# Kernel tuning notes

Hardware: AMD Instinct MI355X
Metric: run time of the kernel (lower is better)

The kernel has to match this reference:

```python
import jax, jax.numpy as jnp
import numpy as np

WS = 7          # window size
NH = 8          # num heads
EPS = 1e-5


def _rel_pos_index(ws):
    # timm WindowAttention relative_position_index, shape (ws*ws, ws*ws), values in [0, (2ws-1)^2)
    coords = np.stack(np.meshgrid(np.arange(ws), np.arange(ws), indexing='ij'))  # 2,ws,ws
    coords = coords.reshape(2, -1)
    rel = coords[:, :, None] - coords[:, None, :]          # 2,N,N
    rel = rel.transpose(1, 2, 0)                           # N,N,2
    rel[:, :, 0] += ws - 1
    rel[:, :, 1] += ws - 1
    rel[:, :, 0] *= 2 * ws - 1
    return rel.sum(-1)                                     # N,N

RPI = jnp.asarray(_rel_pos_index(WS), dtype=jnp.int32)


def _ln(x, g, b):
    mu = jnp.mean(x, axis=-1, keepdims=True)
    var = jnp.mean(jnp.square(x - mu), axis=-1, keepdims=True)
    return (x - mu) * jax.lax.rsqrt(var + EPS) * g + b


def setup_inputs() -> dict:
    key = jax.random.key(0)
    ks = jax.random.split(key, 16)
    C, Hd, V = 256, 1024, 7
    s = lambda k, shp, fan: jax.random.normal(k, shp, jnp.float32) * (fan ** -0.5)
    return {
        'x': jax.random.normal(ks[0], (256, 256, 14, 14), jnp.float32),
        'conv_w': s(ks[1], (C, C), C), 'conv_b': jnp.zeros((C,), jnp.float32),
        'ln1_g': jnp.ones((C,), jnp.float32), 'ln1_b': jnp.zeros((C,), jnp.float32),
        'qkv_w': s(ks[2], (C, 3 * C), C), 'qkv_b': jnp.zeros((3 * C,), jnp.float32),
        'rpb': 0.02 * jax.random.normal(ks[3], ((2 * WS - 1) ** 2, NH), jnp.float32),
        'proj_w': s(ks[4], (C, C), C), 'proj_b': jnp.zeros((C,), jnp.float32),
        'ln2_g': jnp.ones((C,), jnp.float32), 'ln2_b': jnp.zeros((C,), jnp.float32),
        'fc1_w': s(ks[5], (C, Hd), C), 'fc1_b': jnp.zeros((Hd,), jnp.float32),
        'fc2_w': s(ks[6], (Hd, C), Hd), 'fc2_b': jnp.zeros((C,), jnp.float32),
        'fc_out_w': s(ks[7], (C, V), C), 'fc_out_b': jnp.zeros((V,), jnp.float32),
    }


def reference(x, conv_w, conv_b, ln1_g, ln1_b, qkv_w, qkv_b, rpb, proj_w, proj_b,
              ln2_g, ln2_b, fc1_w, fc1_b, fc2_w, fc2_b, fc_out_w, fc_out_b):
    B, Cin, H, W = x.shape
    C = conv_w.shape[0]
    hd = C // NH
    # 1x1 conv projection -> tokens (B, H*W, C)
    t = jnp.einsum('oc,bchw->bhwo', conv_w, x) + conv_b            # B,H,W,C
    tok = t.reshape(B, H * W, C)
    # --- Swin block, shift_size=0 ---
    shortcut = tok
    y = _ln(tok, ln1_g, ln1_b).reshape(B, H, W, C)
    # window partition -> (B*nW, ws*ws, C)
    nHw, nWw = H // WS, W // WS
    yw = y.reshape(B, nHw, WS, nWw, WS, C).transpose(0, 1, 3, 2, 4, 5)
    yw = yw.reshape(B * nHw * nWw, WS * WS, C)
    N = WS * WS
    qkv = (yw @ qkv_w + qkv_b).reshape(-1, N, 3, NH, hd).transpose(2, 0, 3, 1, 4)
    q, k, v = qkv[0], qkv[1], qkv[2]                               # (Bn, NH, N, hd)
    attn = jnp.einsum('bhqd,bhkd->bhqk', q * (hd ** -0.5), k)
    attn = attn + rpb[RPI].transpose(2, 0, 1)[None]                # + (NH,N,N) bias
    attn = jax.nn.softmax(attn, axis=-1)
    o = jnp.einsum('bhqk,bhkd->bqhd', attn, v).reshape(-1, N, C)
    o = o @ proj_w + proj_b
    # window reverse
    o = o.reshape(B, nHw, nWw, WS, WS, C).transpose(0, 1, 3, 2, 4, 5).reshape(B, H * W, C)
    tok = shortcut + o                                             # drop_path = identity (eval)
    h = _ln(tok, ln2_g, ln2_b)
    h = jax.nn.gelu(h @ fc1_w + fc1_b, approximate=False) @ fc2_w + fc2_b
    tok = tok + h
    # global average pool over spatial tokens, then classifier
    pooled = jnp.mean(tok, axis=1)                                 # B,C
    return pooled @ fc_out_w + fc_out_b
```

## Files before the change

kernel.cpp:

```cpp
#include <hip/hip_runtime.h>
#include <math.h>

#define NHEADS 8
#define BATCH  256
#define HWTOK  196
#define MTOT   50176

#define BM 128
#define BN 128
#define BK 64

typedef short bfrag8 __attribute__((ext_vector_type(8)));
typedef float ffrag4 __attribute__((ext_vector_type(4)));

__device__ __forceinline__ unsigned short f2bf(float f) {
  union { float f; unsigned u; } v; v.f = f;
  unsigned r = v.u + 0x7fffu + ((v.u >> 16) & 1u);
  return (unsigned short)(r >> 16);
}
__device__ __forceinline__ float bf2f(unsigned short b) {
  union { unsigned u; float f; } v; v.u = ((unsigned)b) << 16;
  return v.f;
}
__device__ __forceinline__ float bflo(unsigned u) {
  union { unsigned x; float f; } v; v.x = u << 16; return v.f;
}
__device__ __forceinline__ float bfhi(unsigned u) {
  union { unsigned x; float f; } v; v.x = u & 0xffff0000u; return v.f;
}
__device__ __forceinline__ unsigned cvtpk(float a, float b) {
  unsigned r;
  asm("v_cvt_pk_bf16_f32 %0, %1, %2" : "=v"(r) : "v"(a), "v"(b));
  return r;
}
__device__ __forceinline__ float gelu_fast(float x) {
  float ax = fabsf(x);
  float z = ax * 0.70710678118654752f;
  float t = __builtin_amdgcn_rcpf(fmaf(z, 0.3275911f, 1.0f));
  float y = t * (0.254829592f +
            t * (-0.284496736f +
            t * (1.421413741f +
            t * (-1.453152027f +
            t * 1.061405429f))));
  float e2 = __expf(-z * z);
  float erfv = fmaf(-y, e2, 1.0f);
  return 0.5f * fmaf(ax, erfv, x);
}
__device__ __forceinline__ int window_reverse_row(int m) {
  int widx = m / 49, pos = m % 49;
  int b = widx >> 2, wh = (widx >> 1) & 1, ww = widx & 1;
  int i = pos / 7, j = pos % 7;
  return b * 196 + (wh * 7 + i) * 14 + (ww * 7 + j);
}

__device__ __forceinline__ void gload16(const void* g, void* l) {
  __builtin_amdgcn_global_load_lds(
      (const __attribute__((address_space(1))) void*)g,
      (__attribute__((address_space(3))) void*)l, 16, 0, 0);
}

template <int EPI>
__global__ __launch_bounds__(256) void k_gemm_mfma(const unsigned short* __restrict__ A,
                                                   const unsigned short* __restrict__ BT,
                                                   const float* __restrict__ bias,
                                                   void* __restrict__ Cout,
                                                   int rowbase, int N, int K, int nNt) {
  __shared__ __align__(128) unsigned short S[16384];
  const int t = threadIdx.x;
  const int lane = t & 63, w = t >> 6;
  const int wr = w >> 1, wc = w & 1;
  const int cpx = gridDim.x >> 3;
  const int lb = (blockIdx.x & 7) * cpx + (blockIdx.x >> 3);
  const int n_t = lb % nNt, m_t = lb / nNt;
  const int m0 = m_t * BM, n0 = n_t * BN;
  const int l15 = lane & 15;
  const int sw = (lane & 7) << 3;
  const int rA = lane >> 3;
  const int kin = (((lane & 7) ^ rA) << 3);
  ffrag4 acc[4][4] = {};

  for (int k0 = 0; k0 < K; k0 += BK) {
#pragma unroll
    for (int i = 0; i < 4; ++i) {
      const int seg = i * 4 + w;
      const int row = seg * 8 + rA;
      gload16(A + (size_t)(m0 + row) * K + k0 + kin, (char*)S + seg * 1024);
      gload16(BT + (size_t)(n0 + row) * K + k0 + kin, (char*)S + 16384 + seg * 1024);
    }
    __syncthreads();
#pragma unroll
    for (int kk = 0; kk < BK; kk += 32) {
      bfrag8 af[4], bfr[4];
      const int colA = (kk + (lane >> 4) * 8) ^ sw;
#pragma unroll
      for (int mi = 0; mi < 4; ++mi) {
        int row = wr * 64 + mi * 16 + l15;
        af[mi] = *(const bfrag8*)&S[row * BK + colA];
      }
#pragma unroll
      for (int ni = 0; ni < 4; ++ni) {
        int col = wc * 64 + ni * 16 + l15;
        bfr[ni] = *(const bfrag8*)&S[8192 + col * BK + colA];
      }
#pragma unroll
      for (int mi = 0; mi < 4; ++mi)
#pragma unroll
        for (int ni = 0; ni < 4; ++ni)
          acc[mi][ni] = __builtin_amdgcn_mfma_f32_16x16x32_bf16(af[mi], bfr[ni], acc[mi][ni], 0, 0, 0);
    }
    __syncthreads();
  }

  const int cr = (lane >> 4) * 4;
  const int cc = l15;
  float bv[4];
#pragma unroll
  for (int ni = 0; ni < 4; ++ni) bv[ni] = bias[n0 + wc * 64 + ni * 16 + cc];

  float* Sf = (float*)S;
#pragma unroll
  for (int pass = 0; pass < 2; ++pass) {
    if (wr == pass) {
#pragma unroll
      for (int mi = 0; mi < 4; ++mi) {
#pragma unroll
        for (int j = 0; j < 4; ++j) {
          const int mloc = mi * 16 + cr + j;
#pragma unroll
          for (int ni = 0; ni < 4; ++ni) {
            const int nl = wc * 64 + ni * 16 + cc;
            float v = acc[mi][ni][j] + bv[ni];
            if (EPI == 1) v = gelu_fast(v);
            Sf[mloc * 128 + nl] = v;
          }
        }
      }
    }
    __syncthreads();
#pragma unroll
    for (int r = 0; r < 4; ++r) {
      const int flat = (r * 256 + t) * 8;
      const int ml = flat >> 7, nl = flat & 127;
      float4 a = *(const float4*)&Sf[flat];
      float4 b2 = *(const float4*)&Sf[flat + 4];
      uint4 o;
      if (EPI == 2 || EPI == 3) {
        const int gm = rowbase + m0 + pass * 64 + ml;
        const int row = (EPI == 2) ? window_reverse_row(gm) : gm;
        unsigned short* dst = (unsigned short*)Cout + (size_t)row * N + n0 + nl;
        uint4 old = *(const uint4*)dst;
        o.x = cvtpk(bflo(old.x) + a.x, bfhi(old.x) + a.y);
        o.y = cvtpk(bflo(old.y) + a.z, bfhi(old.y) + a.w);
        o.z = cvtpk(bflo(old.z) + b2.x, bfhi(old.z) + b2.y);
        o.w = cvtpk(bflo(old.w) + b2.z, bfhi(old.w) + b2.w);
        *(uint4*)dst = o;
      } else {
        o.x = cvtpk(a.x, a.y);  o.y = cvtpk(a.z, a.w);
        o.z = cvtpk(b2.x, b2.y); o.w = cvtpk(b2.z, b2.w);
        *(uint4*)((unsigned short*)Cout + (size_t)(m0 + pass * 64 + ml) * N + n0 + nl) = o;
      }
    }
    if (pass == 0) __syncthreads();
  }
}

__global__ __launch_bounds__(256) void k_wtrans(const float* __restrict__ w,
                                                unsigned short* __restrict__ wt,
                                                int K, int N) {
  __shared__ float tile[32][33];
  int k0 = blockIdx.x * 32, n0 = blockIdx.y * 32;
  int tx = threadIdx.x & 31, ty = threadIdx.x >> 5;
#pragma unroll
  for (int r = 0; r < 4; ++r)
    tile[ty + r * 8][tx] = w[(size_t)(k0 + ty + r * 8) * N + n0 + tx];
  __syncthreads();
#pragma unroll
  for (int r = 0; r < 4; ++r)
    wt[(size_t)(n0 + ty + r * 8) * K + k0 + tx] = f2bf(tile[tx][ty + r * 8]);
}

__global__ __launch_bounds__(256) void k_cast(const float* __restrict__ w,
                                              unsigned short* __restrict__ wb, int n) {
  int i = blockIdx.x * 256 + threadIdx.x;
  if (i < n) wb[i] = f2bf(w[i]);
}

__global__ __launch_bounds__(256) void k_transpose_x(const float* __restrict__ x,
                                                     unsigned short* __restrict__ xt) {
  __shared__ float tile[32][33];
  int b = blockIdx.x;
  int hw0 = blockIdx.y * 32;
  int c0 = blockIdx.z * 32;
  int tx = threadIdx.x & 31, ty = threadIdx.x >> 5;
#pragma unroll
  for (int r = 0; r < 4; ++r) {
    int c = c0 + ty + r * 8, hw = hw0 + tx;
    if (hw < HWTOK) tile[ty + r * 8][tx] = x[((size_t)b * 256 + c) * HWTOK + hw];
  }
  __syncthreads();
#pragma unroll
  for (int r = 0; r < 4; ++r) {
    int hw = hw0 + ty + r * 8, c = c0 + tx;
    if (hw < HWTOK) xt[((size_t)b * HWTOK + hw) * 256 + c] = f2bf(tile[tx][ty + r * 8]);
  }
}

template <bool WINDOW>
__global__ __launch_bounds__(256) void k_layernorm(const unsigned short* __restrict__ in,
                                                   const float* __restrict__ g,
                                                   const float* __restrict__ bta,
                                                   unsigned short* __restrict__ out,
                                                   int rowbase) {
  int wid = threadIdx.x >> 6, lane = threadIdx.x & 63;
  int li = blockIdx.x * 4 + wid;
  int token = rowbase + li;
  const uint2 xr = *(const uint2*)(in + (size_t)token * 256 + lane * 4);
  float x0 = bflo(xr.x), x1 = bfhi(xr.x), x2 = bflo(xr.y), x3 = bfhi(xr.y);
  float s = x0 + x1 + x2 + x3;
  float sq = x0 * x0 + x1 * x1 + x2 * x2 + x3 * x3;
#pragma unroll
  for (int off = 32; off >= 1; off >>= 1) {
    s += __shfl_xor(s, off);
    sq += __shfl_xor(sq, off);
  }
  float mean = s * (1.f / 256.f);
  float var = sq * (1.f / 256.f) - mean * mean;
  float rstd = rsqrtf(var + 1e-5f);
  float4 gv = *(const float4*)(g + lane * 4);
  float4 bv = *(const float4*)(bta + lane * 4);
  uint2 ov;
  ov.x = cvtpk((x0 - mean) * rstd * gv.x + bv.x,
               (x1 - mean) * rstd * gv.y + bv.y);
  ov.y = cvtpk((x2 - mean) * rstd * gv.z + bv.z,
               (x3 - mean) * rstd * gv.w + bv.w);
  int orow;
  if (WINDOW) {
    int b = token / 196, hw = token % 196;
    int h14 = hw / 14, w14 = hw % 14;
    int wh = h14 / 7, i = h14 % 7, ww = w14 / 7, j = w14 % 7;
    int widx = (b * 2 + wh) * 2 + ww;
    orow = widx * 49 + i * 7 + j - rowbase;
  } else {
    orow = li;
  }
  *(uint2*)(out + (size_t)orow * 256 + lane * 4) = ov;
}

__global__ __launch_bounds__(256) void k_attention(const unsigned short* __restrict__ qkv,
                                                   const float* __restrict__ rpb,
                                                   unsigned short* __restrict__ o) {
  __shared__ unsigned short Kl[4][64 * 40];
  __shared__ unsigned short VTl[4][32 * 72];
  __shared__ unsigned short Pl[4][64 * 72];
  __shared__ float rpbl[4][176];

  const int t = threadIdx.x;
  const int w4 = t >> 6, lane = t & 63;
  const int l15 = lane & 15, g = lane >> 4;
  const int gw = blockIdx.x * 4 + w4;
  const int lw = gw >> 3, head = gw & 7;

  unsigned short* K_ = Kl[w4];
  unsigned short* VT_ = VTl[w4];
  unsigned short* P_ = Pl[w4];
  float* rpb_ = rpbl[w4];

  const size_t baseq = (size_t)lw * 49 * 768 + head * 32;

  for (int e = lane; e < 169; e += 64) rpb_[e] = rpb[e * 8 + head];

  for (int e = lane; e < 512; e += 64) {
    int d = e >> 4, tk = 48 + (e & 15);
    if ((e & 15) != 0) VT_[d * 72 + tk] = 0;
  }

  for (int e = lane; e < 784; e += 64) {
    int tok = e >> 4, dp = e & 15;
    unsigned kv = *(const unsigned*)(qkv + baseq + 256 + (size_t)tok * 768 + dp * 2);
    *(unsigned*)&K_[tok * 40 + dp * 2] = kv;
    unsigned vv = *(const unsigned*)(qkv + baseq + 512 + (size_t)tok * 768 + dp * 2);
    VT_[(dp * 2 + 0) * 72 + tok] = (unsigned short)(vv & 0xffffu);
    VT_[(dp * 2 + 1) * 72 + tok] = (unsigned short)(vv >> 16);
  }

  ffrag4 acc[4][4] = {};
  {
    bfrag8 af[4], bfr[4];
#pragma unroll
    for (int qi = 0; qi < 4; ++qi)
      af[qi] = *(const bfrag8*)(qkv + baseq + (size_t)(16 * qi + l15) * 768 + g * 8);
#pragma unroll
    for (int kj = 0; kj < 4; ++kj)
      bfr[kj] = *(const bfrag8*)&K_[(16 * kj + l15) * 40 + g * 8];
#pragma unroll
    for (int qi = 0; qi < 4; ++qi)
#pragma unroll
      for (int kj = 0; kj < 4; ++kj)
        acc[qi][kj] = __builtin_amdgcn_mfma_f32_16x16x32_bf16(af[qi], bfr[kj], acc[qi][kj], 0, 0, 0);
  }

  const float scale = 0.17677669529663687f;
  int kc[4];
  bool kvalid[4];
#pragma unroll
  for (int kj = 0; kj < 4; ++kj) {
    int c = 16 * kj + l15;
    kc[kj] = 13 * (c / 7) + (c % 7);
    kvalid[kj] = (c < 49);
  }
#pragma unroll
  for (int qi = 0; qi < 4; ++qi) {
#pragma unroll
    for (int j = 0; j < 4; ++j) {
      int q = 16 * qi + 4 * g + j;
      int qc = 13 * (q / 7) + (q % 7);
      float tv[4];
#pragma unroll
      for (int kj = 0; kj < 4; ++kj)
        tv[kj] = kvalid[kj] ? (acc[qi][kj][j] * scale + rpb_[qc - kc[kj] + 84]) : -INFINITY;
      float mx = fmaxf(fmaxf(tv[0], tv[1]), fmaxf(tv[2], tv[3]));
#pragma unroll
      for (int off = 8; off >= 1; off >>= 1) mx = fmaxf(mx, __shfl_xor(mx, off));
      float p[4], sum = 0.f;
#pragma unroll
      for (int kj = 0; kj < 4; ++kj) {
        p[kj] = kvalid[kj] ? __expf(tv[kj] - mx) : 0.f;
        sum += p[kj];
      }
#pragma unroll
      for (int off = 8; off >= 1; off >>= 1) sum += __shfl_xor(sum, off);
      float inv = __builtin_amdgcn_rcpf(sum);
      if (q < 49) {
#pragma unroll
        for (int kj = 0; kj < 4; ++kj)
          P_[q * 72 + 16 * kj + l15] = f2bf(p[kj] * inv);
      }
    }
  }

  ffrag4 accO[2][4] = {};
#pragma unroll
  for (int kk = 0; kk < 64; kk += 32) {
    bfrag8 af2[2], bf2[4];
#pragma unroll
    for (int ti = 0; ti < 2; ++ti)
      af2[ti] = *(const bfrag8*)&VT_[(16 * ti + l15) * 72 + kk + g * 8];
#pragma unroll
    for (int qj = 0; qj < 4; ++qj)
      bf2[qj] = *(const bfrag8*)&P_[(16 * qj + l15) * 72 + kk + g * 8];
#pragma unroll
    for (int ti = 0; ti < 2; ++ti)
#pragma unroll
      for (int qj = 0; qj < 4; ++qj)
        accO[ti][qj] = __builtin_amdgcn_mfma_f32_16x16x32_bf16(af2[ti], bf2[qj], accO[ti][qj], 0, 0, 0);
  }

#pragma unroll
  for (int qj = 0; qj < 4; ++qj) {
    int q = 16 * qj + l15;
    if (q < 49) {
#pragma unroll
      for (int ti = 0; ti < 2; ++ti) {
        uint2 ov;
        ov.x = cvtpk(accO[ti][qj][0], accO[ti][qj][1]);
        ov.y = cvtpk(accO[ti][qj][2], accO[ti][qj][3]);
        *(uint2*)(o + ((size_t)lw * 49 + q) * 256 + head * 32 + 16 * ti + 4 * g) = ov;
      }
    }
  }
}

__global__ __launch_bounds__(256) void k_pool(const unsigned short* __restrict__ tok,
                                              float* __restrict__ pooled) {
  int b = blockIdx.x, c = threadIdx.x;
  float s = 0.f;
  for (int hw = 0; hw < 196; ++hw) s += bf2f(tok[((size_t)b * 196 + hw) * 256 + c]);
  pooled[b * 256 + c] = s * (1.f / 196.f);
}

__global__ __launch_bounds__(64) void k_head(const float* __restrict__ pooled,
                                             const float* __restrict__ w,
                                             const float* __restrict__ bias,
                                             float* __restrict__ out) {
  int b = blockIdx.x, t = threadIdx.x;
  if (t < 7) {
    float s = bias[t];
    for (int c = 0; c < 256; ++c) s = fmaf(pooled[b * 256 + c], w[c * 7 + t], s);
    out[b * 7 + t] = s;
  }
}

extern "C" void kernel_launch(void* const* d_in, const int* in_sizes, int n_in,
                              void* d_out, int out_size, void* d_ws, size_t ws_size,
                              hipStream_t stream) {
  const float* x      = (const float*)d_in[0];
  const float* conv_w = (const float*)d_in[1];
  const float* conv_b = (const float*)d_in[2];
  const float* ln1_g  = (const float*)d_in[3];
  const float* ln1_b  = (const float*)d_in[4];
  const float* qkv_w  = (const float*)d_in[5];
  const float* qkv_b  = (const float*)d_in[6];
  const float* rpb    = (const float*)d_in[7];
  const float* proj_w = (const float*)d_in[8];
  const float* proj_b = (const float*)d_in[9];
  const float* ln2_g  = (const float*)d_in[10];
  const float* ln2_b  = (const float*)d_in[11];
  const float* fc1_w  = (const float*)d_in[12];
  const float* fc1_b  = (const float*)d_in[13];
  const float* fc2_w  = (const float*)d_in[14];
  const float* fc2_b  = (const float*)d_in[15];
  const float* fco_w  = (const float*)d_in[16];
  const float* fco_b  = (const float*)d_in[17];
  float* out = (float*)d_out;
  char* p = (char*)d_ws;

  const size_t FULL_NEED = 182000000ull;
  const int nch = (ws_size >= FULL_NEED) ? 1 : 4;
  const int chw = 1024 / nch;
  const size_t chrows = (size_t)chw * 49;
  const int nMt = (int)(chrows / BM);

  unsigned short* tok = (unsigned short*)p;   p += (size_t)MTOT * 256 * 2;
  unsigned short* Bbuf = (unsigned short*)p;  p += chrows * 1024 * 2;
  unsigned short* Abuf = (unsigned short*)p;  p += chrows * 256 * 2;
  unsigned short* Cbuf = (unsigned short*)p;  p += chrows * 256 * 2;
  unsigned short* cwB  = (unsigned short*)p;  p += 65536 * 2;
  unsigned short* qkvT = (unsigned short*)p;  p += 196608 * 2;
  unsigned short* projT= (unsigned short*)p;  p += 65536 * 2;
  unsigned short* fc1T = (unsigned short*)p;  p += 262144 * 2;
  unsigned short* fc2T = (unsigned short*)p;  p += 262144 * 2;
  float* pool = (float*)p;                    p += 65536 * 4;
  unsigned short* xt = Bbuf;

  k_cast<<<256, 256, 0, stream>>>(conv_w, cwB, 65536);
  k_wtrans<<<dim3(8, 24), 256, 0, stream>>>(qkv_w, qkvT, 256, 768);
  k_wtrans<<<dim3(8, 8), 256, 0, stream>>>(proj_w, projT, 256, 256);
  k_wtrans<<<dim3(8, 32), 256, 0, stream>>>(fc1_w, fc1T, 256, 1024);
  k_wtrans<<<dim3(32, 8), 256, 0, stream>>>(fc2_w, fc2T, 1024, 256);

  k_transpose_x<<<dim3(BATCH, 7, 8), 256, 0, stream>>>(x, xt);
  k_gemm_mfma<0><<<(MTOT / BM) * 2, 256, 0, stream>>>(xt, cwB, conv_b, tok, 0, 256, 256, 2);

  for (int c = 0; c < nch; ++c) {
    const int rowbase = c * (int)chrows;
    k_layernorm<true><<<chrows / 4, 256, 0, stream>>>(tok, ln1_g, ln1_b, Abuf, rowbase);
    k_gemm_mfma<0><<<nMt * 6, 256, 0, stream>>>(Abuf, qkvT, qkv_b, Bbuf, 0, 768, 256, 6);
    k_attention<<<chw * 2, 256, 0, stream>>>(Bbuf, rpb, Cbuf);
    k_gemm_mfma<2><<<nMt * 2, 256, 0, stream>>>(Cbuf, projT, proj_b, tok, rowbase, 256, 256, 2);
    k_layernorm<false><<<chrows / 4, 256, 0, stream>>>(tok, ln2_g, ln2_b, Abuf, rowbase);
    k_gemm_mfma<1><<<nMt * 8, 256, 0, stream>>>(Abuf, fc1T, fc1_b, Bbuf, 0, 1024, 256, 8);
    k_gemm_mfma<3><<<nMt * 2, 256, 0, stream>>>(Bbuf, fc2T, fc2_b, tok, rowbase, 256, 1024, 2);
  }

  k_pool<<<BATCH, 256, 0, stream>>>(tok, pool);
  k_head<<<BATCH, 64, 0, stream>>>(pool, fco_w, fco_b, out);
}
```

Before: 307.4 us.

## Double-buffer GEMM LDS tiles with BK=32 to overlap loads and MFMA

Replaces the single-buffered BK=64 K-loop with two BK=32 LDS buffers, prefetching the next slice while MFMAs run on the current one. The LDS swizzle and load mapping change to fit the 32-wide rows. This is meant to hide global-to-LDS latency behind compute and drop one barrier per tile. The cost is a barrier every 32 K instead of every 64, and less work per iteration to cover latency.

```diff
diff --git a/kernel.cpp b/kernel.cpp
--- a/kernel.cpp
+++ b/kernel.cpp
@@ -8,7 +8,6 @@
 
 #define BM 128
 #define BN 128
-#define BK 64
 
 typedef short bfrag8 __attribute__((ext_vector_type(8)));
 typedef float ffrag4 __attribute__((ext_vector_type(4)));
@@ -74,42 +73,52 @@
   const int n_t = lb % nNt, m_t = lb / nNt;
   const int m0 = m_t * BM, n0 = n_t * BN;
   const int l15 = lane & 15;
-  const int sw = (lane & 7) << 3;
-  const int rA = lane >> 3;
-  const int kin = (((lane & 7) ^ rA) << 3);
+  const int rA = lane >> 2;
+  const int kin = ((lane & 3) ^ ((lane >> 3) & 3)) << 3;
+  const int gA = lane >> 4;
+  const int keyA = (l15 >> 1) & 3;
+  const int colA = ((gA ^ keyA) << 3);
   ffrag4 acc[4][4] = {};
 
-  for (int k0 = 0; k0 < K; k0 += BK) {
-#pragma unroll
-    for (int i = 0; i < 4; ++i) {
-      const int seg = i * 4 + w;
-      const int row = seg * 8 + rA;
-      gload16(A + (size_t)(m0 + row) * K + k0 + kin, (char*)S + seg * 1024);
-      gload16(BT + (size_t)(n0 + row) * K + k0 + kin, (char*)S + 16384 + seg * 1024);
-    }
+#define STAGE(buf, k0_)                                                         \
+  {                                                                             \
+    _Pragma("unroll")                                                           \
+    for (int i = 0; i < 2; ++i) {                                               \
+      const int seg = i * 4 + w;                        \
+      const int row = seg * 16 + rA;                                \
+      gload16(A + (size_t)(m0 + row) * K + (k0_) + kin,                         \
+              (char*)S + (buf) * 8192 + seg * 1024);                            \
+      gload16(BT + (size_t)(n0 + row) * K + (k0_) + kin,                        \
+              (char*)S + 16384 + (buf) * 8192 + seg * 1024);                    \
+    }                                                                           \
+  }
+
+  STAGE(0, 0);
+  __syncthreads();
+  int cur = 0;
+  for (int k0 = 0; k0 < K; k0 += 32) {
+    if (k0 + 32 < K) STAGE(cur ^ 1, k0 + 32);
+    const int ab = cur * 4096, bb = 8192 + cur * 4096;
+    bfrag8 af[4], bfr[4];
+#pragma unroll
+    for (int mi = 0; mi < 4; ++mi) {
+      int row = wr * 64 + mi * 16 + l15;
+      af[mi] = *(const bfrag8*)&S[ab + row * 32 + colA];
+    }
+#pragma unroll
+    for (int ni = 0; ni < 4; ++ni) {
+      int col = wc * 64 + ni * 16 + l15;
+      bfr[ni] = *(const bfrag8*)&S[bb + col * 32 + colA];
+    }
+#pragma unroll
+    for (int mi = 0; mi < 4; ++mi)
+#pragma unroll
+      for (int ni = 0; ni < 4; ++ni)
+        acc[mi][ni] = __builtin_amdgcn_mfma_f32_16x16x32_bf16(af[mi], bfr[ni], acc[mi][ni], 0, 0, 0);
     __syncthreads();
-#pragma unroll
-    for (int kk = 0; kk < BK; kk += 32) {
-      bfrag8 af[4], bfr[4];
-      const int colA = (kk + (lane >> 4) * 8) ^ sw;
-#pragma unroll
-      for (int mi = 0; mi < 4; ++mi) {
-        int row = wr * 64 + mi * 16 + l15;
-        af[mi] = *(const bfrag8*)&S[row * BK + colA];
-      }
-#pragma unroll
-      for (int ni = 0; ni < 4; ++ni) {
-        int col = wc * 64 + ni * 16 + l15;
-        bfr[ni] = *(const bfrag8*)&S[8192 + col * BK + colA];
-      }
-#pragma unroll
-      for (int mi = 0; mi < 4; ++mi)
-#pragma unroll
-        for (int ni = 0; ni < 4; ++ni)
-          acc[mi][ni] = __builtin_amdgcn_mfma_f32_16x16x32_bf16(af[mi], bfr[ni], acc[mi][ni], 0, 0, 0);
-    }
-    __syncthreads();
-  }
+    cur ^= 1;
+  }
+#undef STAGE
 
   const int cr = (lane >> 4) * 4;
   const int cc = l15;
```

Result: no change. 310.8 us (+1.1%).

## Load GEMM MFMA fragments directly from global into registers, bypassing LDS

Applied to the files above, without the earlier changes.

The bf16 GEMM main loop stops staging A and B tiles through LDS with global_load_lds plus barriers. Each wave now loads its MFMA fragments straight from global memory into registers, double-buffering the two 32-wide k halves in software. This removes LDS traffic and the per-iteration __syncthreads, but each tile row is now fetched redundantly by both waves that share it (reuse falls back to L1/L2) and the loads are less coalesced. The barrier between epilogue passes is moved to keep the LDS reuse safe.

```diff
diff --git a/kernel.cpp b/kernel.cpp
--- a/kernel.cpp
+++ b/kernel.cpp
@@ -8,7 +8,6 @@
 
 #define BM 128
 #define BN 128
-#define BK 64
 
 typedef short bfrag8 __attribute__((ext_vector_type(8)));
 typedef float ffrag4 __attribute__((ext_vector_type(4)));
@@ -53,19 +52,13 @@
   return b * 196 + (wh * 7 + i) * 14 + (ww * 7 + j);
 }
 
-__device__ __forceinline__ void gload16(const void* g, void* l) {
-  __builtin_amdgcn_global_load_lds(
-      (const __attribute__((address_space(1))) void*)g,
-      (__attribute__((address_space(3))) void*)l, 16, 0, 0);
-}
-
 template <int EPI>
 __global__ __launch_bounds__(256) void k_gemm_mfma(const unsigned short* __restrict__ A,
                                                    const unsigned short* __restrict__ BT,
                                                    const float* __restrict__ bias,
                                                    void* __restrict__ Cout,
                                                    int rowbase, int N, int K, int nNt) {
-  __shared__ __align__(128) unsigned short S[16384];
+  __shared__ __align__(128) float Sf[8192];
   const int t = threadIdx.x;
   const int lane = t & 63, w = t >> 6;
   const int wr = w >> 1, wc = w & 1;
@@ -73,42 +66,47 @@
   const int lb = (blockIdx.x & 7) * cpx + (blockIdx.x >> 3);
   const int n_t = lb % nNt, m_t = lb / nNt;
   const int m0 = m_t * BM, n0 = n_t * BN;
-  const int l15 = lane & 15;
-  const int sw = (lane & 7) << 3;
-  const int rA = lane >> 3;
-  const int kin = (((lane & 7) ^ rA) << 3);
+  const int l15 = lane & 15, g = lane >> 4;
   ffrag4 acc[4][4] = {};
 
-  for (int k0 = 0; k0 < K; k0 += BK) {
+  const unsigned short* Ap[4];
+  const unsigned short* Bp[4];
+#pragma unroll
+  for (int mi = 0; mi < 4; ++mi)
+    Ap[mi] = A + (size_t)(m0 + wr * 64 + mi * 16 + l15) * K + g * 8;
+#pragma unroll
+  for (int ni = 0; ni < 4; ++ni)
+    Bp[ni] = BT + (size_t)(n0 + wc * 64 + ni * 16 + l15) * K + g * 8;
+
+  bfrag8 a0[4], b0[4], a1[4], b1[4];
+#pragma unroll
+  for (int i = 0; i < 4; ++i) {
+    a0[i] = *(const bfrag8*)(Ap[i]);
+    b0[i] = *(const bfrag8*)(Bp[i]);
+  }
+  for (int k0 = 0; k0 < K; k0 += 64) {
 #pragma unroll
     for (int i = 0; i < 4; ++i) {
-      const int seg = i * 4 + w;
-      const int row = seg * 8 + rA;
-      gload16(A + (size_t)(m0 + row) * K + k0 + kin, (char*)S + seg * 1024);
-      gload16(BT + (size_t)(n0 + row) * K + k0 + kin, (char*)S + 16384 + seg * 1024);
-    }
-    __syncthreads();
-#pragma unroll
-    for (int kk = 0; kk < BK; kk += 32) {
-      bfrag8 af[4], bfr[4];
-      const int colA = (kk + (lane >> 4) * 8) ^ sw;
-#pragma unroll
-      for (int mi = 0; mi < 4; ++mi) {
-        int row = wr * 64 + mi * 16 + l15;
-        af[mi] = *(const bfrag8*)&S[row * BK + colA];
-      }
-#pragma unroll
-      for (int ni = 0; ni < 4; ++ni) {
-        int col = wc * 64 + ni * 16 + l15;
-        bfr[ni] = *(const bfrag8*)&S[8192 + col * BK + colA];
-      }
-#pragma unroll
-      for (int mi = 0; mi < 4; ++mi)
-#pragma unroll
-        for (int ni = 0; ni < 4; ++ni)
-          acc[mi][ni] = __builtin_amdgcn_mfma_f32_16x16x32_bf16(af[mi], bfr[ni], acc[mi][ni], 0, 0, 0);
-    }
-    __syncthreads();
+      a1[i] = *(const bfrag8*)(Ap[i] + k0 + 32);
+      b1[i] = *(const bfrag8*)(Bp[i] + k0 + 32);
+    }
+#pragma unroll
+    for (int mi = 0; mi < 4; ++mi)
+#pragma unroll
+      for (int ni = 0; ni < 4; ++ni)
+        acc[mi][ni] = __builtin_amdgcn_mfma_f32_16x16x32_bf16(a0[mi], b0[ni], acc[mi][ni], 0, 0, 0);
+    if (k0 + 64 < K) {
+#pragma unroll
+      for (int i = 0; i < 4; ++i) {
+        a0[i] = *(const bfrag8*)(Ap[i] + k0 + 64);
+        b0[i] = *(const bfrag8*)(Bp[i] + k0 + 64);
+      }
+    }
+#pragma unroll
+    for (int mi = 0; mi < 4; ++mi)
+#pragma unroll
+      for (int ni = 0; ni < 4; ++ni)
+        acc[mi][ni] = __builtin_amdgcn_mfma_f32_16x16x32_bf16(a1[mi], b1[ni], acc[mi][ni], 0, 0, 0);
   }
 
   const int cr = (lane >> 4) * 4;
@@ -117,9 +115,9 @@
 #pragma unroll
   for (int ni = 0; ni < 4; ++ni) bv[ni] = bias[n0 + wc * 64 + ni * 16 + cc];
 
-  float* Sf = (float*)S;
 #pragma unroll
   for (int pass = 0; pass < 2; ++pass) {
+    if (pass == 1) __syncthreads();
     if (wr == pass) {
 #pragma unroll
       for (int mi = 0; mi < 4; ++mi) {
@@ -160,7 +158,6 @@
         *(uint4*)((unsigned short*)Cout + (size_t)(m0 + pass * 64 + ml) * N + n0 + nl) = o;
       }
     }
-    if (pass == 0) __syncthreads();
   }
 }
 
```

Result: slower. 499.1 us (+62.4%).

## Fuse fc1+GELU+fc2 into a single MLP kernel keeping hidden activations in LDS

Applied to the files above, without the earlier changes.

Replaces the separate fc1 (with GELU epilogue) and fc2 GEMM launches with one kernel per 128-row tile. Each 128-column hidden chunk is computed, passed through GELU, stored as bf16 in LDS, and immediately consumed by the fc2 accumulation, so the 1024-wide hidden tensor never goes to global memory. It also adds an XCD block swizzle helper that falls back when the grid is not a multiple of 8. The cost is 128KB of LDS and one block per CU with no double buffering, which lowers occupancy and latency hiding, and each block reloads all fc1 and fc2 weights.

```diff
diff --git a/kernel.cpp b/kernel.cpp
--- a/kernel.cpp
+++ b/kernel.cpp
@@ -59,6 +59,11 @@
       (__attribute__((address_space(3))) void*)l, 16, 0, 0);
 }
 
+__device__ __forceinline__ int xcd_swz() {
+  if (gridDim.x & 7) return (int)blockIdx.x;
+  return (int)((blockIdx.x & 7) * (gridDim.x >> 3) + (blockIdx.x >> 3));
+}
+
 template <int EPI>
 __global__ __launch_bounds__(256) void k_gemm_mfma(const unsigned short* __restrict__ A,
                                                    const unsigned short* __restrict__ BT,
@@ -69,8 +74,7 @@
   const int t = threadIdx.x;
   const int lane = t & 63, w = t >> 6;
   const int wr = w >> 1, wc = w & 1;
-  const int cpx = gridDim.x >> 3;
-  const int lb = (blockIdx.x & 7) * cpx + (blockIdx.x >> 3);
+  const int lb = xcd_swz();
   const int n_t = lb % nNt, m_t = lb / nNt;
   const int m0 = m_t * BM, n0 = n_t * BN;
   const int l15 = lane & 15;
@@ -129,9 +133,7 @@
 #pragma unroll
           for (int ni = 0; ni < 4; ++ni) {
             const int nl = wc * 64 + ni * 16 + cc;
-            float v = acc[mi][ni][j] + bv[ni];
-            if (EPI == 1) v = gelu_fast(v);
-            Sf[mloc * 128 + nl] = v;
+            Sf[mloc * 128 + nl] = acc[mi][ni][j] + bv[ni];
           }
         }
       }
@@ -159,6 +161,162 @@
         o.z = cvtpk(b2.x, b2.y); o.w = cvtpk(b2.z, b2.w);
         *(uint4*)((unsigned short*)Cout + (size_t)(m0 + pass * 64 + ml) * N + n0 + nl) = o;
       }
+    }
+    if (pass == 0) __syncthreads();
+  }
+}
+
+__global__ __launch_bounds__(256, 1) void k_mlp(const unsigned short* __restrict__ A,
+                                                const unsigned short* __restrict__ fc1T,
+                                                const unsigned short* __restrict__ fc2T,
+                                                const float* __restrict__ b1g,
+                                                const float* __restrict__ b2g,
+                                                unsigned short* __restrict__ tok,
+                                                int rowbase) {
+  __shared__ __align__(128) char S[131072];
+  unsigned short* Al = (unsigned short*)S;
+  unsigned short* Bl = (unsigned short*)(S + 65536);
+  unsigned short* Cl = (unsigned short*)(S + 98304);
+
+  const int t = threadIdx.x;
+  const int lane = t & 63, w = t >> 6;
+  const int wr = w >> 1, wc = w & 1;
+  const int l15 = lane & 15, g = lane >> 4;
+  const int key = lane & 7;
+  const int cr = (lane >> 4) * 4, cc = l15;
+  const int m0 = xcd_swz() * 128;
+
+  ffrag4 acc2[4][8] = {};
+
+#pragma unroll
+  for (int i = 0; i < 16; ++i) {
+    const int inst = i * 4 + w;
+    const int r = inst * 2 + (lane >> 5);
+    const int sg = ((lane & 31) ^ (r & 7)) << 3;
+    gload16(A + (size_t)(m0 + r) * 256 + sg, (char*)Al + inst * 1024);
+  }
+
+  for (int hc = 0; hc < 8; ++hc) {
+    float b1[4];
+#pragma unroll
+    for (int ni = 0; ni < 4; ++ni)
+      b1[ni] = b1g[hc * 128 + wc * 64 + ni * 16 + cc];
+
+    ffrag4 acch[4][4] = {};
+#pragma unroll
+    for (int p = 0; p < 2; ++p) {
+      __syncthreads();
+#pragma unroll
+      for (int i = 0; i < 8; ++i) {
+        const int inst = i * 4 + w;
+        const int r = inst * 4 + (lane >> 4);
+        const int sg = p * 128 + (((lane & 15) ^ (r & 7)) << 3);
+        gload16(fc1T + (size_t)(hc * 128 + r) * 256 + sg, (char*)Bl + inst * 1024);
+      }
+      __syncthreads();
+#pragma unroll
+      for (int kk = 0; kk < 128; kk += 32) {
+        bfrag8 af[4], bf[4];
+        const int qA = ((p * 16 + (kk >> 3) + g) ^ key) << 3;
+        const int qB = (((kk >> 3) + g) ^ key) << 3;
+#pragma unroll
+        for (int mi = 0; mi < 4; ++mi)
+          af[mi] = *(const bfrag8*)&Al[(wr * 64 + mi * 16 + l15) * 256 + qA];
+#pragma unroll
+        for (int ni = 0; ni < 4; ++ni)
+          bf[ni] = *(const bfrag8*)&Bl[(wc * 64 + ni * 16 + l15) * 128 + qB];
+#pragma unroll
+        for (int mi = 0; mi < 4; ++mi)
+#pragma unroll
+          for (int ni = 0; ni < 4; ++ni)
+            acch[mi][ni] = __builtin_amdgcn_mfma_f32_16x16x32_bf16(af[mi], bf[ni], acch[mi][ni], 0, 0, 0);
+      }
+    }
+    __syncthreads();
+
+#pragma unroll
+    for (int mi = 0; mi < 4; ++mi) {
+#pragma unroll
+      for (int j = 0; j < 4; ++j) {
+        const int row = wr * 64 + mi * 16 + cr + j;
+        const int k8 = (row & 7) << 3;
+#pragma unroll
+        for (int ni = 0; ni < 4; ++ni) {
+          const int col = wc * 64 + ni * 16 + cc;
+          Cl[row * 128 + (col ^ k8)] = f2bf(gelu_fast(acch[mi][ni][j] + b1[ni]));
+        }
+      }
+    }
+
+#pragma unroll
+    for (int h = 0; h < 2; ++h) {
+      if (h == 1) __syncthreads();
+#pragma unroll
+      for (int i = 0; i < 8; ++i) {
+        const int inst = i * 4 + w;
+        const int r = inst * 8 + (lane >> 3);
+        const int sg = hc * 128 + h * 64 + (((lane & 7) ^ (r & 7)) << 3);
+        gload16(fc2T + (size_t)r * 1024 + sg, (char*)Bl + inst * 1024);
+      }
+      __syncthreads();
+#pragma unroll
+      for (int kk2 = 0; kk2 < 64; kk2 += 32) {
+        bfrag8 af2[4], bf2[8];
+        const int qC = ((h * 8 + (kk2 >> 3) + g) ^ key) << 3;
+        const int qB2 = (((kk2 >> 3) + g) ^ key) << 3;
+#pragma unroll
+        for (int mi = 0; mi < 4; ++mi)
+          af2[mi] = *(const bfrag8*)&Cl[(wr * 64 + mi * 16 + l15) * 128 + qC];
+#pragma unroll
+        for (int ni = 0; ni < 8; ++ni)
+          bf2[ni] = *(const bfrag8*)&Bl[(wc * 128 + ni * 16 + l15) * 64 + qB2];
+#pragma unroll
+        for (int mi = 0; mi < 4; ++mi)
+#pragma unroll
+          for (int ni = 0; ni < 8; ++ni)
+            acc2[mi][ni] = __builtin_amdgcn_mfma_f32_16x16x32_bf16(af2[mi], bf2[ni], acc2[mi][ni], 0, 0, 0);
+      }
+    }
+  }
+
+  __syncthreads();
+  float b2v[8];
+#pragma unroll
+  for (int ni = 0; ni < 8; ++ni) b2v[ni] = b2g[wc * 128 + ni * 16 + cc];
+
+  float* Sf = (float*)S;
+#pragma unroll
+  for (int pass = 0; pass < 2; ++pass) {
+    if (wr == pass) {
+#pragma unroll
+      for (int mi = 0; mi < 4; ++mi) {
+#pragma unroll
+        for (int j = 0; j < 4; ++j) {
+          const int mloc = mi * 16 + cr + j;
+#pragma unroll
+          for (int ni = 0; ni < 8; ++ni) {
+            const int nl = wc * 128 + ni * 16 + cc;
+            Sf[mloc * 256 + nl] = acc2[mi][ni][j] + b2v[ni];
+          }
+        }
+      }
+    }
+    __syncthreads();
+#pragma unroll
+    for (int r = 0; r < 8; ++r) {
+      const int flat = (r * 256 + t) * 8;
+      const int ml = flat >> 8, nl = flat & 255;
+      float4 a = *(const float4*)&Sf[flat];
+      float4 b = *(const float4*)&Sf[flat + 4];
+      const int gm = rowbase + m0 + pass * 64 + ml;
+      unsigned short* dst = tok + (size_t)gm * 256 + nl;
+      uint4 old = *(const uint4*)dst;
+      uint4 o;
+      o.x = cvtpk(bflo(old.x) + a.x, bfhi(old.x) + a.y);
+      o.y = cvtpk(bflo(old.y) + a.z, bfhi(old.y) + a.w);
+      o.z = cvtpk(bflo(old.z) + b.x, bfhi(old.z) + b.y);
+      o.w = cvtpk(bflo(old.w) + b.z, bfhi(old.w) + b.w);
+      *(uint4*)dst = o;
     }
     if (pass == 0) __syncthreads();
   }
@@ -448,8 +606,7 @@
     k_attention<<<chw * 2, 256, 0, stream>>>(Bbuf, rpb, Cbuf);
     k_gemm_mfma<2><<<nMt * 2, 256, 0, stream>>>(Cbuf, projT, proj_b, tok, rowbase, 256, 256, 2);
     k_layernorm<false><<<chrows / 4, 256, 0, stream>>>(tok, ln2_g, ln2_b, Abuf, rowbase);
-    k_gemm_mfma<1><<<nMt * 8, 256, 0, stream>>>(Abuf, fc1T, fc1_b, Bbuf, 0, 1024, 256, 8);
-    k_gemm_mfma<3><<<nMt * 2, 256, 0, stream>>>(Bbuf, fc2T, fc2_b, tok, rowbase, 256, 1024, 2);
+    k_mlp<<<nMt, 256, 0, stream>>>(Abuf, fc1T, fc2T, fc1_b, fc2_b, tok, rowbase);
   }
 
   k_pool<<<BATCH, 256, 0, stream>>>(tok, pool);
```

Result: slower. 337.5 us (+9.8%).
